# Kernel optimization log

Measured on AMD Instinct MI355X. Metric: run time of the kernel, lower is better.

The kernel has to match this reference:

```python
import jax, jax.numpy as jnp
import numpy as np

B, K, D_IN, H, CTX, RH = 4096, 4, 1024, 1024, 256, 64
TEMP, MIN_MOD = 1.0, 2
LN_EPS = 1e-5


def setup_inputs() -> dict:
    key = jax.random.key(0)
    ks = jax.random.split(key, 8)
    nrm = lambda i, shape, scale: jax.random.normal(ks[i], shape, jnp.float32) * scale
    return {
        "context": jax.random.normal(ks[0], (B, CTX), jnp.float32),
        "x": jax.random.normal(ks[1], (K, B, D_IN), jnp.float32),  # stacked modality inputs
        # Gumbel noise, matching -log(-log(U + 1e-8) + 1e-8)
        "gumbel": -jnp.log(-jnp.log(jax.random.uniform(ks[2], (B, K), jnp.float32) + 1e-8) + 1e-8),
        # router MLP params
        "W1": nrm(3, (CTX, RH), 1.0 / np.sqrt(CTX)), "b1": jnp.zeros((RH,), jnp.float32),
        "g_ln": jnp.ones((RH,), jnp.float32), "beta_ln": jnp.zeros((RH,), jnp.float32),
        "W2": nrm(4, (RH, RH // 2), 1.0 / np.sqrt(RH)), "b2": jnp.zeros((RH // 2,), jnp.float32),
        "W3": nrm(5, (RH // 2, K), 1.0 / np.sqrt(RH // 2)), "b3": jnp.zeros((K,), jnp.float32),
        "prior": jnp.zeros((K,), jnp.float32),
        # per-modality linear encoders (stacked)
        "W_enc": nrm(6, (K, D_IN, H), 1.0 / np.sqrt(D_IN)), "b_enc": jnp.zeros((K, H), jnp.float32),
        "fusion_w": jnp.ones((K,), jnp.float32),
    }


def reference(context, x, gumbel, W1, b1, g_ln, beta_ln, W2, b2, W3, b3,
              prior, W_enc, b_enc, fusion_w):
    # --- router MLP: Linear -> LayerNorm -> ReLU -> Linear -> ReLU -> Linear ---
    h = context @ W1 + b1                                   # [B, RH]
    mu = h.mean(-1, keepdims=True)
    var = h.var(-1, keepdims=True)
    h = (h - mu) / jnp.sqrt(var + LN_EPS) * g_ln + beta_ln
    h = jax.nn.relu(h)
    h = jax.nn.relu(h @ W2 + b2)                            # [B, RH//2]
    logits = h @ W3 + b3 + prior                            # [B, K]
    probs = jax.nn.sigmoid(logits)
    # Gumbel-sigmoid soft selection (training path)
    soft = jax.nn.sigmoid((logits + gumbel) / TEMP)
    # force top-min_modalities on
    _, top_idx = jax.lax.top_k(probs, MIN_MOD)              # [B, MIN_MOD]
    rows = jnp.arange(probs.shape[0])[:, None]
    min_mask = jnp.zeros_like(probs).at[rows, top_idx].set(1.0)
    mask = jnp.maximum(soft, min_mask)                      # [B, K]
    # --- conditional encoders: run only where mask > 0.5 (equiv: compute + zero) ---
    enc = jnp.einsum('kbd,kdh->bkh', x, W_enc) + b_enc[None, :, :]   # [B, K, H]
    hard = (mask > 0.5).astype(enc.dtype)                   # gather/scatter indicator
    enc = enc * hard[..., None] * mask[..., None]           # zero-fill + soft gating
    # --- fusion (softmax-weighted sum over modalities) ---
    w = jax.nn.softmax(fusion_w)                            # [K]
    fused = jnp.einsum('bkh,k->bh', enc, w)                 # [B, H]
    return fused
```

## Files before the change

### kernel.cpp

```cpp
#include <hip/hip_runtime.h>
#include <hip/hip_bf16.h>

#define NB    4096
#define NK    4
#define ND    1024
#define NH    1024
#define NCTX  256
#define NRH   64

typedef float f32x4 __attribute__((ext_vector_type(4)));
typedef float f32x8 __attribute__((ext_vector_type(8)));
typedef short s16x8 __attribute__((ext_vector_type(8)));
typedef __bf16 bf16x8 __attribute__((ext_vector_type(8)));

__device__ __forceinline__ unsigned short f2bf_rne(float f) {
    unsigned int u = __float_as_uint(f);
    u += 0x7fffu + ((u >> 16) & 1u);
    return (unsigned short)(u >> 16);
}
__device__ __forceinline__ float bf2f(unsigned short s) {
    return __uint_as_float(((unsigned int)s) << 16);
}
__device__ __forceinline__ void gl_lds16(const void* g, void* l) {
    __builtin_amdgcn_global_load_lds(
        (const __attribute__((address_space(1))) unsigned int*)g,
        (__attribute__((address_space(3))) unsigned int*)l, 16, 0, 0);
}

__global__ __launch_bounds__(256) void router_k(
    const float* __restrict__ ctx, const float* __restrict__ gum,
    const float* __restrict__ W1, const float* __restrict__ b1,
    const float* __restrict__ gln, const float* __restrict__ bln,
    const float* __restrict__ W2, const float* __restrict__ b2,
    const float* __restrict__ W3, const float* __restrict__ b3,
    const float* __restrict__ prior, const float* __restrict__ fw,
    float* __restrict__ gates)
{
    __shared__ float sH[4][4][64];
    __shared__ float sH2[4][4][32];

    const int tid  = threadIdx.x;
    const int w    = tid >> 6;
    const int lane = tid & 63;
    const int rowbase = blockIdx.x * 16 + w * 4;
    const int rbu = __builtin_amdgcn_readfirstlane(rowbase);
    const float* c0 = ctx + (size_t)rbu * NCTX;

    float a0 = 0.f, a1 = 0.f, a2 = 0.f, a3 = 0.f;
#pragma unroll 8
    for (int d = 0; d < NCTX; ++d) {
        float wv = W1[d * NRH + lane];
        a0 = fmaf(c0[d],          wv, a0);
        a1 = fmaf(c0[NCTX + d],   wv, a1);
        a2 = fmaf(c0[2*NCTX + d], wv, a2);
        a3 = fmaf(c0[3*NCTX + d], wv, a3);
    }
    const float bb = b1[lane];
    float hr[4] = {a0 + bb, a1 + bb, a2 + bb, a3 + bb};
    const float gl = gln[lane], be = bln[lane];

#pragma unroll
    for (int r = 0; r < 4; ++r) {
        float h = hr[r];
        float s = h;
#pragma unroll
        for (int m = 32; m >= 1; m >>= 1) s += __shfl_xor(s, m);
        float mu = s * (1.f / 64.f);
        float dd = h - mu;
        float q = dd * dd;
#pragma unroll
        for (int m = 32; m >= 1; m >>= 1) q += __shfl_xor(q, m);
        float var = q * (1.f / 64.f);
        h = dd * rsqrtf(var + 1e-5f) * gl + be;
        sH[w][r][lane] = fmaxf(h, 0.f);
    }

#pragma unroll
    for (int p = 0; p < 2; ++p) {
        const int r = p * 2 + (lane >> 5);
        const int j = lane & 31;
        float acc = b2[j];
#pragma unroll 8
        for (int l = 0; l < 64; ++l)
            acc = fmaf(sH[w][r][l], W2[l * 32 + j], acc);
        sH2[w][r][j] = fmaxf(acc, 0.f);
    }

    const int r3 = lane >> 2, j3 = lane & 3;
    float lg = 0.f;
    if (lane < 16) {
        lg = b3[j3] + prior[j3];
#pragma unroll 8
        for (int l = 0; l < 32; ++l)
            lg = fmaf(sH2[w][r3][l], W3[l * 4 + j3], lg);
    }
    float pj = 1.f / (1.f + expf(-lg));
    const int base = lane & 60;
    float P0 = __shfl(pj, base), P1 = __shfl(pj, base | 1);
    float P2 = __shfl(pj, base | 2), P3 = __shfl(pj, base | 3);

    if (lane < 16) {
        float f0 = fw[0], f1 = fw[1], f2 = fw[2], f3 = fw[3];
        float fm = fmaxf(fmaxf(f0, f1), fmaxf(f2, f3));
        float e0 = expf(f0 - fm), e1 = expf(f1 - fm), e2 = expf(f2 - fm), e3 = expf(f3 - fm);
        float es = e0 + e1 + e2 + e3;
        float wsm = (j3 == 0 ? e0 : j3 == 1 ? e1 : j3 == 2 ? e2 : e3) / es;

        int cnt = 0;
        cnt += (P0 > pj) || ((P0 == pj) && (0 < j3));
        cnt += (P1 > pj) || ((P1 == pj) && (1 < j3));
        cnt += (P2 > pj) || ((P2 == pj) && (2 < j3));
        cnt += (P3 > pj) || ((P3 == pj) && (3 < j3));

        const int row = rowbase + r3;
        float soft = 1.f / (1.f + expf(-(lg + gum[row * 4 + j3])));
        float mask = (cnt < 2) ? 1.0f : soft;
        float gate = (mask > 0.5f) ? mask * wsm : 0.0f;
        gates[row * 4 + j3] = gate;
    }
}

__global__ __launch_bounds__(256) void wprep_k(
    const float* __restrict__ W, unsigned short* __restrict__ whi,
    unsigned short* __restrict__ wlo)
{
    __shared__ float sT[32][33];
    const int bid = blockIdx.x;
    const int k  = bid >> 10;
    const int dt = (bid >> 5) & 31;
    const int ht = bid & 31;
    const int t = threadIdx.x;
    {
        const int r  = t >> 3;
        const int c4 = (t & 7) << 2;
        const float* src = W + ((size_t)k << 20) + (size_t)(dt * 32 + r) * 1024 + (ht * 32 + c4);
        float4 v = *(const float4*)src;
        sT[c4 + 0][r] = v.x; sT[c4 + 1][r] = v.y;
        sT[c4 + 2][r] = v.z; sT[c4 + 3][r] = v.w;
    }
    __syncthreads();
    {
        const int h  = t >> 3;
        const int d4 = (t & 7) << 2;
        float u0 = sT[h][d4], u1 = sT[h][d4 + 1], u2 = sT[h][d4 + 2], u3 = sT[h][d4 + 3];
        ushort4 uh, ul;
        uh.x = f2bf_rne(u0); ul.x = f2bf_rne(u0 - bf2f(uh.x));
        uh.y = f2bf_rne(u1); ul.y = f2bf_rne(u1 - bf2f(uh.y));
        uh.z = f2bf_rne(u2); ul.z = f2bf_rne(u2 - bf2f(uh.z));
        uh.w = f2bf_rne(u3); ul.w = f2bf_rne(u3 - bf2f(uh.w));
        size_t o = ((size_t)k << 20) + (size_t)(ht * 32 + h) * 1024 + (dt * 32 + d4);
        *(ushort4*)(whi + o) = uh;
        *(ushort4*)(wlo + o) = ul;
    }
}

__global__ __launch_bounds__(256) void aprep_k(
    const float* __restrict__ x, const float* __restrict__ gates,
    unsigned short* __restrict__ Ah, unsigned short* __restrict__ Al)
{
    const int bid = blockIdx.x;
    const int k  = bid >> 11;
    const int bp = bid & 2047;
    const int t = threadIdx.x;
    const int boff = t >> 7;
    const int d8 = (t & 127) << 3;
    const int b = bp * 2 + boff;
    const float g = gates[b * 4 + k];

    f32x8 v = *(const f32x8*)(x + ((size_t)k << 22) + (size_t)b * ND + d8);
    v *= g;
    bf16x8 hb = __builtin_convertvector(v, bf16x8);
    f32x8  hf = __builtin_convertvector(hb, f32x8);
    bf16x8 lb = __builtin_convertvector(v - hf, bf16x8);
    const size_t o = (size_t)b * 4096 + (k << 10) + d8;
    *(s16x8*)(Ah + o) = __builtin_bit_cast(s16x8, hb);
    *(s16x8*)(Al + o) = __builtin_bit_cast(s16x8, lb);
}

__global__ __launch_bounds__(256, 3) void gemm_k(
    const unsigned short* __restrict__ Ahg, const unsigned short* __restrict__ Alg,
    const unsigned short* __restrict__ Bhg, const unsigned short* __restrict__ Blg,
    const float* __restrict__ gates, const float* __restrict__ benc,
    float* __restrict__ out)
{
    __shared__ unsigned short sAh[128 * 64];
    __shared__ unsigned short sAl[128 * 64];
    __shared__ unsigned short sBh[64 * 64];
    __shared__ unsigned short sBl[64 * 64];

    const int bid = blockIdx.x;
    const int wg  = (bid & 7) * 64 + (bid >> 3);
    const int bm  = wg >> 4;
    const int bn  = wg & 15;

    const int tid = threadIdx.x;
    const int wv  = tid >> 6, ln = tid & 63;
    const int wr  = wv >> 1,  wc = wv & 1;
    const int l15 = ln & 15,  ls = ln >> 4;
    const int rowb = bm * 128;
    const int colb = bn * 64;

    const int srow = ln >> 3;
    const int slot = (ln & 7) ^ srow;
    size_t aoff[4];
#pragma unroll
    for (int i = 0; i < 4; ++i) {
        const int row = (wv * 4 + i) * 8 + srow;
        aoff[i] = (size_t)(rowb + row) * 4096 + slot * 8;
    }
    size_t boff[2];
#pragma unroll
    for (int i = 0; i < 2; ++i) {
        const int row = (wv * 2 + i) * 8 + srow;
        boff[i] = (size_t)(colb + row) * 1024 + slot * 8;
    }

    const int arow0 = (wr * 64 + l15) * 128;
    const int brow0 = (wc * 32 + l15) * 128;
    const int xr = (l15 & 7) << 4;
    int colswz[2];
#pragma unroll
    for (int kk = 0; kk < 2; ++kk)
        colswz[kk] = ((kk << 6) + (ls << 4)) ^ xr;

    f32x4 acc[4][2];
#pragma unroll
    for (int a = 0; a < 4; ++a)
#pragma unroll
        for (int b = 0; b < 2; ++b)
            acc[a][b] = (f32x4){0.f, 0.f, 0.f, 0.f};

#pragma unroll 1
    for (int kt = 0; kt < 64; ++kt) {
        const int kbase = kt * 64;
        const size_t wkoff = ((size_t)(kt >> 4) << 20) + (size_t)(kt & 15) * 64;

#pragma unroll
        for (int i = 0; i < 4; ++i) {
            const int chunk = wv * 4 + i;
            gl_lds16(Ahg + aoff[i] + kbase, &sAh[chunk * 512]);
            gl_lds16(Alg + aoff[i] + kbase, &sAl[chunk * 512]);
        }
#pragma unroll
        for (int i = 0; i < 2; ++i) {
            const int chunk = wv * 2 + i;
            gl_lds16(Bhg + boff[i] + wkoff, &sBh[chunk * 512]);
            gl_lds16(Blg + boff[i] + wkoff, &sBl[chunk * 512]);
        }
        __syncthreads();

#pragma unroll
        for (int kk = 0; kk < 2; ++kk) {
            s16x8 ah[4], al[4], bh[2], bl[2];
#pragma unroll
            for (int mi = 0; mi < 4; ++mi) {
                const int ab = arow0 + mi * 2048 + colswz[kk];
                ah[mi] = *(const s16x8*)((const char*)sAh + ab);
                al[mi] = *(const s16x8*)((const char*)sAl + ab);
            }
#pragma unroll
            for (int ni = 0; ni < 2; ++ni) {
                const int bb = brow0 + ni * 2048 + colswz[kk];
                bh[ni] = *(const s16x8*)((const char*)sBh + bb);
                bl[ni] = *(const s16x8*)((const char*)sBl + bb);
            }
#pragma unroll
            for (int mi = 0; mi < 4; ++mi)
#pragma unroll
                for (int ni = 0; ni < 2; ++ni)
                    acc[mi][ni] = __builtin_amdgcn_mfma_f32_16x16x32_bf16(
                        ah[mi], bh[ni], acc[mi][ni], 0, 0, 0);
#pragma unroll
            for (int mi = 0; mi < 4; ++mi)
#pragma unroll
                for (int ni = 0; ni < 2; ++ni)
                    acc[mi][ni] = __builtin_amdgcn_mfma_f32_16x16x32_bf16(
                        ah[mi], bl[ni], acc[mi][ni], 0, 0, 0);
#pragma unroll
            for (int mi = 0; mi < 4; ++mi)
#pragma unroll
                for (int ni = 0; ni < 2; ++ni)
                    acc[mi][ni] = __builtin_amdgcn_mfma_f32_16x16x32_bf16(
                        al[mi], bh[ni], acc[mi][ni], 0, 0, 0);
        }
        __syncthreads();
    }

    float bce[2][4];
#pragma unroll
    for (int ni = 0; ni < 2; ++ni) {
        const int col = colb + wc * 32 + ni * 16 + l15;
#pragma unroll
        for (int kk = 0; kk < 4; ++kk)
            bce[ni][kk] = benc[kk * NH + col];
    }
#pragma unroll
    for (int mi = 0; mi < 4; ++mi) {
#pragma unroll
        for (int j = 0; j < 4; ++j) {
            const int row = rowb + wr * 64 + mi * 16 + ls * 4 + j;
            const float4 g = *(const float4*)(gates + row * 4);
#pragma unroll
            for (int ni = 0; ni < 2; ++ni) {
                const int col = colb + wc * 32 + ni * 16 + l15;
                float bias = g.x * bce[ni][0] + g.y * bce[ni][1] +
                             g.z * bce[ni][2] + g.w * bce[ni][3];
                out[(size_t)row * NH + col] = acc[mi][ni][j] + bias;
            }
        }
    }
}

extern "C" void kernel_launch(void* const* d_in, const int* in_sizes, int n_in,
                              void* d_out, int out_size, void* d_ws, size_t ws_size,
                              hipStream_t stream)
{
    const float* ctx   = (const float*)d_in[0];
    const float* x     = (const float*)d_in[1];
    const float* gum   = (const float*)d_in[2];
    const float* W1    = (const float*)d_in[3];
    const float* b1    = (const float*)d_in[4];
    const float* gln   = (const float*)d_in[5];
    const float* bln   = (const float*)d_in[6];
    const float* W2    = (const float*)d_in[7];
    const float* b2    = (const float*)d_in[8];
    const float* W3    = (const float*)d_in[9];
    const float* b3    = (const float*)d_in[10];
    const float* prior = (const float*)d_in[11];
    const float* Wenc  = (const float*)d_in[12];
    const float* benc  = (const float*)d_in[13];
    const float* fw    = (const float*)d_in[14];
    float* out = (float*)d_out;

    char* ws = (char*)d_ws;
    float* gates        = (float*)ws;
    unsigned short* bh  = (unsigned short*)(ws + (64 << 10));
    unsigned short* bl  = (unsigned short*)(ws + (64 << 10) + (8ull << 20));
    unsigned short* ah  = (unsigned short*)(ws + (64 << 10) + (16ull << 20));
    unsigned short* al  = (unsigned short*)(ws + (64 << 10) + (48ull << 20));

    hipLaunchKernelGGL(router_k, dim3(256), dim3(256), 0, stream,
                       ctx, gum, W1, b1, gln, bln, W2, b2, W3, b3, prior, fw, gates);
    hipLaunchKernelGGL(aprep_k, dim3(8192), dim3(256), 0, stream, x, gates, ah, al);
    hipLaunchKernelGGL(wprep_k, dim3(4096), dim3(256), 0, stream, Wenc, bh, bl);
    hipLaunchKernelGGL(gemm_k, dim3(512), dim3(256), 0, stream,
                       ah, al, bh, bl, gates, benc, out);
}
```

Measured before the change: 264.9 us.

## Switch split-precision GEMM to fp16 with scaled residual and double-buffered LDS

```diff
diff --git a/kernel.cpp b/kernel.cpp
--- a/kernel.cpp
+++ b/kernel.cpp
@@ -11,16 +11,11 @@
 typedef float f32x4 __attribute__((ext_vector_type(4)));
 typedef float f32x8 __attribute__((ext_vector_type(8)));
 typedef short s16x8 __attribute__((ext_vector_type(8)));
-typedef __bf16 bf16x8 __attribute__((ext_vector_type(8)));
-
-__device__ __forceinline__ unsigned short f2bf_rne(float f) {
-    unsigned int u = __float_as_uint(f);
-    u += 0x7fffu + ((u >> 16) & 1u);
-    return (unsigned short)(u >> 16);
-}
-__device__ __forceinline__ float bf2f(unsigned short s) {
-    return __uint_as_float(((unsigned int)s) << 16);
-}
+typedef _Float16 f16x8 __attribute__((ext_vector_type(8)));
+
+#define RES_SCALE 2048.0f
+#define RES_INV   (1.0f/2048.0f)
+
 __device__ __forceinline__ void gl_lds16(const void* g, void* l) {
     __builtin_amdgcn_global_load_lds(
         (const __attribute__((address_space(1))) unsigned int*)g,
@@ -142,21 +137,24 @@
     {
         const int h  = t >> 3;
         const int d4 = (t & 7) << 2;
-        float u0 = sT[h][d4], u1 = sT[h][d4 + 1], u2 = sT[h][d4 + 2], u3 = sT[h][d4 + 3];
-        ushort4 uh, ul;
-        uh.x = f2bf_rne(u0); ul.x = f2bf_rne(u0 - bf2f(uh.x));
-        uh.y = f2bf_rne(u1); ul.y = f2bf_rne(u1 - bf2f(uh.y));
-        uh.z = f2bf_rne(u2); ul.z = f2bf_rne(u2 - bf2f(uh.z));
-        uh.w = f2bf_rne(u3); ul.w = f2bf_rne(u3 - bf2f(uh.w));
+        unsigned short uh[4], ul[4];
+#pragma unroll
+        for (int q = 0; q < 4; ++q) {
+            float u = sT[h][d4 + q];
+            _Float16 hi = (_Float16)u;
+            _Float16 lo = (_Float16)((u - (float)hi) * RES_SCALE);
+            uh[q] = __builtin_bit_cast(unsigned short, hi);
+            ul[q] = __builtin_bit_cast(unsigned short, lo);
+        }
         size_t o = ((size_t)k << 20) + (size_t)(ht * 32 + h) * 1024 + (dt * 32 + d4);
-        *(ushort4*)(whi + o) = uh;
-        *(ushort4*)(wlo + o) = ul;
+        *(ushort4*)(whi + o) = make_ushort4(uh[0], uh[1], uh[2], uh[3]);
+        *(ushort4*)(wlo + o) = make_ushort4(ul[0], ul[1], ul[2], ul[3]);
     }
 }
 
 __global__ __launch_bounds__(256) void aprep_k(
     const float* __restrict__ x, const float* __restrict__ gates,
-    unsigned short* __restrict__ Ah, unsigned short* __restrict__ Al)
+    unsigned short* __restrict__ Ah)
 {
     const int bid = blockIdx.x;
     const int k  = bid >> 11;
@@ -169,24 +167,20 @@
 
     f32x8 v = *(const f32x8*)(x + ((size_t)k << 22) + (size_t)b * ND + d8);
     v *= g;
-    bf16x8 hb = __builtin_convertvector(v, bf16x8);
-    f32x8  hf = __builtin_convertvector(hb, f32x8);
-    bf16x8 lb = __builtin_convertvector(v - hf, bf16x8);
+    f16x8 hb = __builtin_convertvector(v, f16x8);
     const size_t o = (size_t)b * 4096 + (k << 10) + d8;
     *(s16x8*)(Ah + o) = __builtin_bit_cast(s16x8, hb);
-    *(s16x8*)(Al + o) = __builtin_bit_cast(s16x8, lb);
-}
-
-__global__ __launch_bounds__(256, 3) void gemm_k(
-    const unsigned short* __restrict__ Ahg, const unsigned short* __restrict__ Alg,
+}
+
+__global__ __launch_bounds__(256, 2) void gemm_k(
+    const unsigned short* __restrict__ Ahg,
     const unsigned short* __restrict__ Bhg, const unsigned short* __restrict__ Blg,
     const float* __restrict__ gates, const float* __restrict__ benc,
     float* __restrict__ out)
 {
-    __shared__ unsigned short sAh[128 * 64];
-    __shared__ unsigned short sAl[128 * 64];
-    __shared__ unsigned short sBh[64 * 64];
-    __shared__ unsigned short sBl[64 * 64];
+    __shared__ unsigned short sA0[128 * 64], sA1[128 * 64];
+    __shared__ unsigned short sBh0[64 * 64], sBh1[64 * 64];
+    __shared__ unsigned short sBl0[64 * 64], sBl1[64 * 64];
 
     const int bid = blockIdx.x;
     const int wg  = (bid & 7) * 64 + (bid >> 3);
@@ -223,68 +217,72 @@
     for (int kk = 0; kk < 2; ++kk)
         colswz[kk] = ((kk << 6) + (ls << 4)) ^ xr;
 
-    f32x4 acc[4][2];
+    f32x4 acch[4][2], accl[4][2];
 #pragma unroll
     for (int a = 0; a < 4; ++a)
 #pragma unroll
-        for (int b = 0; b < 2; ++b)
-            acc[a][b] = (f32x4){0.f, 0.f, 0.f, 0.f};
+        for (int b = 0; b < 2; ++b) {
+            acch[a][b] = (f32x4){0.f, 0.f, 0.f, 0.f};
+            accl[a][b] = (f32x4){0.f, 0.f, 0.f, 0.f};
+        }
+
+#define STAGE(SA, SBH, SBL, KT)                                               \
+    do {                                                                      \
+        const int kb_ = (KT) * 64;                                            \
+        const size_t wk_ = ((size_t)((KT) >> 4) << 20) + (size_t)((KT) & 15) * 64; \
+        _Pragma("unroll")                                                     \
+        for (int i = 0; i < 4; ++i)                                           \
+            gl_lds16(Ahg + aoff[i] + kb_, &(SA)[(wv * 4 + i) * 512]);         \
+        _Pragma("unroll")                                                     \
+        for (int i = 0; i < 2; ++i) {                                         \
+            gl_lds16(Bhg + boff[i] + wk_, &(SBH)[(wv * 2 + i) * 512]);        \
+            gl_lds16(Blg + boff[i] + wk_, &(SBL)[(wv * 2 + i) * 512]);        \
+        }                                                                     \
+    } while (0)
+
+#define COMPUTE(SA, SBH, SBL)                                                 \
+    do {                                                                      \
+        _Pragma("unroll")                                                     \
+        for (int kk = 0; kk < 2; ++kk) {                                      \
+            f16x8 ah[4], bh[2], bl[2];                                        \
+            _Pragma("unroll")                                                 \
+            for (int mi = 0; mi < 4; ++mi)                                    \
+                ah[mi] = __builtin_bit_cast(f16x8, *(const s16x8*)((const char*)(SA) + arow0 + mi * 2048 + colswz[kk])); \
+            _Pragma("unroll")                                                 \
+            for (int ni = 0; ni < 2; ++ni) {                                  \
+                bh[ni] = __builtin_bit_cast(f16x8, *(const s16x8*)((const char*)(SBH) + brow0 + ni * 2048 + colswz[kk])); \
+                bl[ni] = __builtin_bit_cast(f16x8, *(const s16x8*)((const char*)(SBL) + brow0 + ni * 2048 + colswz[kk])); \
+            }                                                                 \
+            _Pragma("unroll")                                                 \
+            for (int mi = 0; mi < 4; ++mi)                                    \
+                _Pragma("unroll")                                             \
+                for (int ni = 0; ni < 2; ++ni)                                \
+                    acch[mi][ni] = __builtin_amdgcn_mfma_f32_16x16x32_f16(    \
+                        ah[mi], bh[ni], acch[mi][ni], 0, 0, 0);               \
+            _Pragma("unroll")                                                 \
+            for (int mi = 0; mi < 4; ++mi)                                    \
+                _Pragma("unroll")                                             \
+                for (int ni = 0; ni < 2; ++ni)                                \
+                    accl[mi][ni] = __builtin_amdgcn_mfma_f32_16x16x32_f16(    \
+                        ah[mi], bl[ni], accl[mi][ni], 0, 0, 0);               \
+        }                                                                     \
+    } while (0)
+
+    STAGE(sA0, sBh0, sBl0, 0);
+    __syncthreads();
 
 #pragma unroll 1
-    for (int kt = 0; kt < 64; ++kt) {
-        const int kbase = kt * 64;
-        const size_t wkoff = ((size_t)(kt >> 4) << 20) + (size_t)(kt & 15) * 64;
-
-#pragma unroll
-        for (int i = 0; i < 4; ++i) {
-            const int chunk = wv * 4 + i;
-            gl_lds16(Ahg + aoff[i] + kbase, &sAh[chunk * 512]);
-            gl_lds16(Alg + aoff[i] + kbase, &sAl[chunk * 512]);
-        }
-#pragma unroll
-        for (int i = 0; i < 2; ++i) {
-            const int chunk = wv * 2 + i;
-            gl_lds16(Bhg + boff[i] + wkoff, &sBh[chunk * 512]);
-            gl_lds16(Blg + boff[i] + wkoff, &sBl[chunk * 512]);
-        }
+    for (int kt = 0; kt < 64; kt += 2) {
+        STAGE(sA1, sBh1, sBl1, kt + 1);
+        COMPUTE(sA0, sBh0, sBl0);
         __syncthreads();
-
-#pragma unroll
-        for (int kk = 0; kk < 2; ++kk) {
-            s16x8 ah[4], al[4], bh[2], bl[2];
-#pragma unroll
-            for (int mi = 0; mi < 4; ++mi) {
-                const int ab = arow0 + mi * 2048 + colswz[kk];
-                ah[mi] = *(const s16x8*)((const char*)sAh + ab);
-                al[mi] = *(const s16x8*)((const char*)sAl + ab);
-            }
-#pragma unroll
-            for (int ni = 0; ni < 2; ++ni) {
-                const int bb = brow0 + ni * 2048 + colswz[kk];
-                bh[ni] = *(const s16x8*)((const char*)sBh + bb);
-                bl[ni] = *(const s16x8*)((const char*)sBl + bb);
-            }
-#pragma unroll
-            for (int mi = 0; mi < 4; ++mi)
-#pragma unroll
-                for (int ni = 0; ni < 2; ++ni)
-                    acc[mi][ni] = __builtin_amdgcn_mfma_f32_16x16x32_bf16(
-                        ah[mi], bh[ni], acc[mi][ni], 0, 0, 0);
-#pragma unroll
-            for (int mi = 0; mi < 4; ++mi)
-#pragma unroll
-                for (int ni = 0; ni < 2; ++ni)
-                    acc[mi][ni] = __builtin_amdgcn_mfma_f32_16x16x32_bf16(
-                        ah[mi], bl[ni], acc[mi][ni], 0, 0, 0);
-#pragma unroll
-            for (int mi = 0; mi < 4; ++mi)
-#pragma unroll
-                for (int ni = 0; ni < 2; ++ni)
-                    acc[mi][ni] = __builtin_amdgcn_mfma_f32_16x16x32_bf16(
-                        al[mi], bh[ni], acc[mi][ni], 0, 0, 0);
-        }
+        if (kt + 2 < 64)
+            STAGE(sA0, sBh0, sBl0, kt + 2);
+        COMPUTE(sA1, sBh1, sBl1);
         __syncthreads();
     }
+#undef STAGE
+#undef COMPUTE
 
     float bce[2][4];
 #pragma unroll
@@ -305,7 +303,8 @@
                 const int col = colb + wc * 32 + ni * 16 + l15;
                 float bias = g.x * bce[ni][0] + g.y * bce[ni][1] +
                              g.z * bce[ni][2] + g.w * bce[ni][3];
-                out[(size_t)row * NH + col] = acc[mi][ni][j] + bias;
+                out[(size_t)row * NH + col] =
+                    acch[mi][ni][j] + accl[mi][ni][j] * RES_INV + bias;
             }
         }
     }
@@ -337,12 +336,11 @@
     unsigned short* bh  = (unsigned short*)(ws + (64 << 10));
     unsigned short* bl  = (unsigned short*)(ws + (64 << 10) + (8ull << 20));
     unsigned short* ah  = (unsigned short*)(ws + (64 << 10) + (16ull << 20));
-    unsigned short* al  = (unsigned short*)(ws + (64 << 10) + (48ull << 20));
 
     hipLaunchKernelGGL(router_k, dim3(256), dim3(256), 0, stream,
                        ctx, gum, W1, b1, gln, bln, W2, b2, W3, b3, prior, fw, gates);
-    hipLaunchKernelGGL(aprep_k, dim3(8192), dim3(256), 0, stream, x, gates, ah, al);
+    hipLaunchKernelGGL(aprep_k, dim3(8192), dim3(256), 0, stream, x, gates, ah);
     hipLaunchKernelGGL(wprep_k, dim3(4096), dim3(256), 0, stream, Wenc, bh, bl);
     hipLaunchKernelGGL(gemm_k, dim3(512), dim3(256), 0, stream,
-                       ah, al, bh, bl, gates, benc, out);
-}
+                       ah, bh, bl, gates, benc, out);
+}
```

After: 225.3 us. 1.18x faster.

## Replace split-bf16 three-pass GEMM with single fp16 MFMA and split-K atomics

Applied to the files above, without the earlier changes.

```diff
diff --git a/kernel.cpp b/kernel.cpp
--- a/kernel.cpp
+++ b/kernel.cpp
@@ -11,16 +11,8 @@
 typedef float f32x4 __attribute__((ext_vector_type(4)));
 typedef float f32x8 __attribute__((ext_vector_type(8)));
 typedef short s16x8 __attribute__((ext_vector_type(8)));
-typedef __bf16 bf16x8 __attribute__((ext_vector_type(8)));
-
-__device__ __forceinline__ unsigned short f2bf_rne(float f) {
-    unsigned int u = __float_as_uint(f);
-    u += 0x7fffu + ((u >> 16) & 1u);
-    return (unsigned short)(u >> 16);
-}
-__device__ __forceinline__ float bf2f(unsigned short s) {
-    return __uint_as_float(((unsigned int)s) << 16);
-}
+typedef _Float16 f16x8 __attribute__((ext_vector_type(8)));
+
 __device__ __forceinline__ void gl_lds16(const void* g, void* l) {
     __builtin_amdgcn_global_load_lds(
         (const __attribute__((address_space(1))) unsigned int*)g,
@@ -121,8 +113,7 @@
 }
 
 __global__ __launch_bounds__(256) void wprep_k(
-    const float* __restrict__ W, unsigned short* __restrict__ whi,
-    unsigned short* __restrict__ wlo)
+    const float* __restrict__ W, unsigned short* __restrict__ whi)
 {
     __shared__ float sT[32][33];
     const int bid = blockIdx.x;
@@ -142,21 +133,20 @@
     {
         const int h  = t >> 3;
         const int d4 = (t & 7) << 2;
-        float u0 = sT[h][d4], u1 = sT[h][d4 + 1], u2 = sT[h][d4 + 2], u3 = sT[h][d4 + 3];
-        ushort4 uh, ul;
-        uh.x = f2bf_rne(u0); ul.x = f2bf_rne(u0 - bf2f(uh.x));
-        uh.y = f2bf_rne(u1); ul.y = f2bf_rne(u1 - bf2f(uh.y));
-        uh.z = f2bf_rne(u2); ul.z = f2bf_rne(u2 - bf2f(uh.z));
-        uh.w = f2bf_rne(u3); ul.w = f2bf_rne(u3 - bf2f(uh.w));
+        unsigned short uh[4];
+#pragma unroll
+        for (int q = 0; q < 4; ++q) {
+            _Float16 hi = (_Float16)sT[h][d4 + q];
+            uh[q] = __builtin_bit_cast(unsigned short, hi);
+        }
         size_t o = ((size_t)k << 20) + (size_t)(ht * 32 + h) * 1024 + (dt * 32 + d4);
-        *(ushort4*)(whi + o) = uh;
-        *(ushort4*)(wlo + o) = ul;
+        *(ushort4*)(whi + o) = make_ushort4(uh[0], uh[1], uh[2], uh[3]);
     }
 }
 
 __global__ __launch_bounds__(256) void aprep_k(
     const float* __restrict__ x, const float* __restrict__ gates,
-    unsigned short* __restrict__ Ah, unsigned short* __restrict__ Al)
+    unsigned short* __restrict__ Ah)
 {
     const int bid = blockIdx.x;
     const int k  = bid >> 11;
@@ -169,130 +159,108 @@
 
     f32x8 v = *(const f32x8*)(x + ((size_t)k << 22) + (size_t)b * ND + d8);
     v *= g;
-    bf16x8 hb = __builtin_convertvector(v, bf16x8);
-    f32x8  hf = __builtin_convertvector(hb, f32x8);
-    bf16x8 lb = __builtin_convertvector(v - hf, bf16x8);
+    f16x8 hb = __builtin_convertvector(v, f16x8);
     const size_t o = (size_t)b * 4096 + (k << 10) + d8;
     *(s16x8*)(Ah + o) = __builtin_bit_cast(s16x8, hb);
-    *(s16x8*)(Al + o) = __builtin_bit_cast(s16x8, lb);
-}
-
-__global__ __launch_bounds__(256, 3) void gemm_k(
-    const unsigned short* __restrict__ Ahg, const unsigned short* __restrict__ Alg,
-    const unsigned short* __restrict__ Bhg, const unsigned short* __restrict__ Blg,
+}
+
+__global__ __launch_bounds__(256) void zero_k(float* __restrict__ out)
+{
+    const size_t i = ((size_t)blockIdx.x * 256 + threadIdx.x) * 8;
+    *(f32x8*)(out + i) = (f32x8){0.f,0.f,0.f,0.f,0.f,0.f,0.f,0.f};
+}
+
+__global__ __launch_bounds__(256, 2) void gemm_k(
+    const unsigned short* __restrict__ Ahg,
+    const unsigned short* __restrict__ Bhg,
     const float* __restrict__ gates, const float* __restrict__ benc,
     float* __restrict__ out)
 {
-    __shared__ unsigned short sAh[128 * 64];
-    __shared__ unsigned short sAl[128 * 64];
-    __shared__ unsigned short sBh[64 * 64];
-    __shared__ unsigned short sBl[64 * 64];
+    __shared__ unsigned short sA[128 * 64];
+    __shared__ unsigned short sB[128 * 64];
 
     const int bid = blockIdx.x;
     const int wg  = (bid & 7) * 64 + (bid >> 3);
-    const int bm  = wg >> 4;
-    const int bn  = wg & 15;
+    const int ksp = wg >> 8;
+    const int rem = wg & 255;
+    const int bm  = rem >> 3;
+    const int bn  = rem & 7;
 
     const int tid = threadIdx.x;
     const int wv  = tid >> 6, ln = tid & 63;
     const int wr  = wv >> 1,  wc = wv & 1;
     const int l15 = ln & 15,  ls = ln >> 4;
     const int rowb = bm * 128;
-    const int colb = bn * 64;
+    const int colb = bn * 128;
 
     const int srow = ln >> 3;
     const int slot = (ln & 7) ^ srow;
-    size_t aoff[4];
+    size_t aoff[4], boff[4];
 #pragma unroll
     for (int i = 0; i < 4; ++i) {
         const int row = (wv * 4 + i) * 8 + srow;
         aoff[i] = (size_t)(rowb + row) * 4096 + slot * 8;
-    }
-    size_t boff[2];
-#pragma unroll
-    for (int i = 0; i < 2; ++i) {
-        const int row = (wv * 2 + i) * 8 + srow;
         boff[i] = (size_t)(colb + row) * 1024 + slot * 8;
     }
 
     const int arow0 = (wr * 64 + l15) * 128;
-    const int brow0 = (wc * 32 + l15) * 128;
+    const int brow0 = (wc * 64 + l15) * 128;
     const int xr = (l15 & 7) << 4;
     int colswz[2];
 #pragma unroll
     for (int kk = 0; kk < 2; ++kk)
         colswz[kk] = ((kk << 6) + (ls << 4)) ^ xr;
 
-    f32x4 acc[4][2];
+    f32x4 acc[4][4];
 #pragma unroll
     for (int a = 0; a < 4; ++a)
 #pragma unroll
-        for (int b = 0; b < 2; ++b)
+        for (int b = 0; b < 4; ++b)
             acc[a][b] = (f32x4){0.f, 0.f, 0.f, 0.f};
 
 #pragma unroll 1
-    for (int kt = 0; kt < 64; ++kt) {
-        const int kbase = kt * 64;
-        const size_t wkoff = ((size_t)(kt >> 4) << 20) + (size_t)(kt & 15) * 64;
+    for (int kt = 0; kt < 32; ++kt) {
+        const int kflat = ksp * 2048 + kt * 64;
+        const size_t wk = ((size_t)(kflat >> 10) << 20) + (size_t)(kflat & 1023);
 
 #pragma unroll
         for (int i = 0; i < 4; ++i) {
             const int chunk = wv * 4 + i;
-            gl_lds16(Ahg + aoff[i] + kbase, &sAh[chunk * 512]);
-            gl_lds16(Alg + aoff[i] + kbase, &sAl[chunk * 512]);
-        }
-#pragma unroll
-        for (int i = 0; i < 2; ++i) {
-            const int chunk = wv * 2 + i;
-            gl_lds16(Bhg + boff[i] + wkoff, &sBh[chunk * 512]);
-            gl_lds16(Blg + boff[i] + wkoff, &sBl[chunk * 512]);
+            gl_lds16(Ahg + aoff[i] + kflat, &sA[chunk * 512]);
+            gl_lds16(Bhg + boff[i] + wk,    &sB[chunk * 512]);
         }
         __syncthreads();
 
 #pragma unroll
         for (int kk = 0; kk < 2; ++kk) {
-            s16x8 ah[4], al[4], bh[2], bl[2];
-#pragma unroll
-            for (int mi = 0; mi < 4; ++mi) {
-                const int ab = arow0 + mi * 2048 + colswz[kk];
-                ah[mi] = *(const s16x8*)((const char*)sAh + ab);
-                al[mi] = *(const s16x8*)((const char*)sAl + ab);
-            }
-#pragma unroll
-            for (int ni = 0; ni < 2; ++ni) {
-                const int bb = brow0 + ni * 2048 + colswz[kk];
-                bh[ni] = *(const s16x8*)((const char*)sBh + bb);
-                bl[ni] = *(const s16x8*)((const char*)sBl + bb);
-            }
+            f16x8 af[4], bf[4];
 #pragma unroll
             for (int mi = 0; mi < 4; ++mi)
-#pragma unroll
-                for (int ni = 0; ni < 2; ++ni)
-                    acc[mi][ni] = __builtin_amdgcn_mfma_f32_16x16x32_bf16(
-                        ah[mi], bh[ni], acc[mi][ni], 0, 0, 0);
+                af[mi] = __builtin_bit_cast(f16x8,
+                    *(const s16x8*)((const char*)sA + arow0 + mi * 2048 + colswz[kk]));
+#pragma unroll
+            for (int ni = 0; ni < 4; ++ni)
+                bf[ni] = __builtin_bit_cast(f16x8,
+                    *(const s16x8*)((const char*)sB + brow0 + ni * 2048 + colswz[kk]));
 #pragma unroll
             for (int mi = 0; mi < 4; ++mi)
 #pragma unroll
-                for (int ni = 0; ni < 2; ++ni)
-                    acc[mi][ni] = __builtin_amdgcn_mfma_f32_16x16x32_bf16(
-                        ah[mi], bl[ni], acc[mi][ni], 0, 0, 0);
-#pragma unroll
-            for (int mi = 0; mi < 4; ++mi)
-#pragma unroll
-                for (int ni = 0; ni < 2; ++ni)
-                    acc[mi][ni] = __builtin_amdgcn_mfma_f32_16x16x32_bf16(
-                        al[mi], bh[ni], acc[mi][ni], 0, 0, 0);
+                for (int ni = 0; ni < 4; ++ni)
+                    acc[mi][ni] = __builtin_amdgcn_mfma_f32_16x16x32_f16(
+                        af[mi], bf[ni], acc[mi][ni], 0, 0, 0);
         }
         __syncthreads();
     }
 
-    float bce[2][4];
-#pragma unroll
-    for (int ni = 0; ni < 2; ++ni) {
-        const int col = colb + wc * 32 + ni * 16 + l15;
-#pragma unroll
-        for (int kk = 0; kk < 4; ++kk)
-            bce[ni][kk] = benc[kk * NH + col];
+    float bce[4][4];
+    if (ksp == 0) {
+#pragma unroll
+        for (int ni = 0; ni < 4; ++ni) {
+            const int col = colb + wc * 64 + ni * 16 + l15;
+#pragma unroll
+            for (int kk = 0; kk < 4; ++kk)
+                bce[ni][kk] = benc[kk * NH + col];
+        }
     }
 #pragma unroll
     for (int mi = 0; mi < 4; ++mi) {
@@ -301,11 +269,13 @@
             const int row = rowb + wr * 64 + mi * 16 + ls * 4 + j;
             const float4 g = *(const float4*)(gates + row * 4);
 #pragma unroll
-            for (int ni = 0; ni < 2; ++ni) {
-                const int col = colb + wc * 32 + ni * 16 + l15;
-                float bias = g.x * bce[ni][0] + g.y * bce[ni][1] +
-                             g.z * bce[ni][2] + g.w * bce[ni][3];
-                out[(size_t)row * NH + col] = acc[mi][ni][j] + bias;
+            for (int ni = 0; ni < 4; ++ni) {
+                const int col = colb + wc * 64 + ni * 16 + l15;
+                float val = acc[mi][ni][j];
+                if (ksp == 0)
+                    val += g.x * bce[ni][0] + g.y * bce[ni][1] +
+                           g.z * bce[ni][2] + g.w * bce[ni][3];
+                unsafeAtomicAdd(out + (size_t)row * NH + col, val);
             }
         }
     }
@@ -335,14 +305,13 @@
     char* ws = (char*)d_ws;
     float* gates        = (float*)ws;
     unsigned short* bh  = (unsigned short*)(ws + (64 << 10));
-    unsigned short* bl  = (unsigned short*)(ws + (64 << 10) + (8ull << 20));
-    unsigned short* ah  = (unsigned short*)(ws + (64 << 10) + (16ull << 20));
-    unsigned short* al  = (unsigned short*)(ws + (64 << 10) + (48ull << 20));
+    unsigned short* ah  = (unsigned short*)(ws + (64 << 10) + (8ull << 20));
 
     hipLaunchKernelGGL(router_k, dim3(256), dim3(256), 0, stream,
                        ctx, gum, W1, b1, gln, bln, W2, b2, W3, b3, prior, fw, gates);
-    hipLaunchKernelGGL(aprep_k, dim3(8192), dim3(256), 0, stream, x, gates, ah, al);
-    hipLaunchKernelGGL(wprep_k, dim3(4096), dim3(256), 0, stream, Wenc, bh, bl);
+    hipLaunchKernelGGL(aprep_k, dim3(8192), dim3(256), 0, stream, x, gates, ah);
+    hipLaunchKernelGGL(wprep_k, dim3(4096), dim3(256), 0, stream, Wenc, bh);
+    hipLaunchKernelGGL(zero_k, dim3(2048), dim3(256), 0, stream, out);
     hipLaunchKernelGGL(gemm_k, dim3(512), dim3(256), 0, stream,
-                       ah, al, bh, bl, gates, benc, out);
-}
+                       ah, bh, gates, benc, out);
+}
```

Result: faster. 231.3 us (-12.7%).
